# Performance work log

Measured on AMD Instinct MI355X. Metric: run time of the kernel, lower is better.

The kernel has to match this reference:

```python
import jax, jax.numpy as jnp
import numpy as np

B, S, D, H = 2, 2048, 1024, 16
DK = D // H


def setup_inputs() -> dict:
    key = jax.random.key(0)
    ks = jax.random.split(key, 11)
    scale = 1.0 / np.sqrt(D)
    inp = {
        "query": jax.random.normal(ks[0], (B, S, D), dtype=jnp.float32),
        "key": jax.random.normal(ks[1], (B, S, D), dtype=jnp.float32),
        "value": jax.random.normal(ks[2], (B, S, D), dtype=jnp.float32),
        "Wq": jax.random.normal(ks[3], (D, D), dtype=jnp.float32) * scale,
        "bq": jnp.zeros((D,), dtype=jnp.float32),
        "Wk": jax.random.normal(ks[4], (D, D), dtype=jnp.float32) * scale,
        "bk": jnp.zeros((D,), dtype=jnp.float32),
        "Wv": jax.random.normal(ks[5], (D, D), dtype=jnp.float32) * scale,
        "bv": jnp.zeros((D,), dtype=jnp.float32),
        "Wo": jax.random.normal(ks[6], (D, D), dtype=jnp.float32) * scale,
        "bo": jnp.zeros((D,), dtype=jnp.float32),
    }
    return inp


def _split_heads(x):
    # [B,S,D] -> [B,H,S,DK]
    b, s, _ = x.shape
    return x.reshape(b, s, H, DK).transpose(0, 2, 1, 3)


def reference(query, key, value, Wq, bq, Wk, bk, Wv, bv, Wo, bo):
    q = _split_heads(query @ Wq.T + bq)
    k = _split_heads(key @ Wk.T + bk)
    v = _split_heads(value @ Wv.T + bv)
    # scaled dot-product attention: [B,H,S,S]
    scores = jnp.einsum("bhqd,bhkd->bhqk", q, k) / np.sqrt(DK).astype(np.float32)
    attn = jax.nn.softmax(scores, axis=-1)  # stable max-subtract softmax, same math
    ctx = jnp.einsum("bhqk,bhkd->bhqd", attn, v)  # [B,H,S,DK]
    ctx = ctx.transpose(0, 2, 1, 3).reshape(query.shape[0], -1, H * DK)
    return ctx @ Wo.T + bo
```

## Files before the change

kernel.cpp:

```cpp
#include <hip/hip_runtime.h>
#include <math.h>

constexpr int NB = 2;
constexpr int NS = 2048;
constexpr int ND = 1024;
constexpr int NH = 16;
constexpr int NDK = 64;

typedef __attribute__((ext_vector_type(8))) short short8;
typedef __attribute__((ext_vector_type(4))) float floatx4;

__device__ inline unsigned short f2bf(float x) {
    unsigned u = __builtin_bit_cast(unsigned, x);
    u += 0x7fffu + ((u >> 16) & 1u);
    return (unsigned short)(u >> 16);
}

#define GLOAD_LDS16(g, l) __builtin_amdgcn_global_load_lds( \
    (const __attribute__((address_space(1))) void*)(g),     \
    (__attribute__((address_space(3))) void*)(l), 16, 0, 0)

#define QSCALE 0.18033688f

__global__ __launch_bounds__(256) void cvt3(
    const float* __restrict__ s0, const float* __restrict__ s1,
    const float* __restrict__ s2,
    unsigned short* __restrict__ d0, unsigned short* __restrict__ d1,
    unsigned short* __restrict__ d2)
{
    const float* s = (blockIdx.y == 0) ? s0 : (blockIdx.y == 1) ? s1 : s2;
    unsigned short* d = (blockIdx.y == 0) ? d0 : (blockIdx.y == 1) ? d1 : d2;
    int i = (blockIdx.x * 256 + threadIdx.x) * 8;
    float4 a = *(const float4*)(s + i);
    float4 b = *(const float4*)(s + i + 4);
    unsigned short t[8] = {f2bf(a.x), f2bf(a.y), f2bf(a.z), f2bf(a.w),
                           f2bf(b.x), f2bf(b.y), f2bf(b.z), f2bf(b.w)};
    *(uint4*)(d + i) = *(uint4*)t;
}

__global__ __launch_bounds__(256) void cvt4(
    const float* __restrict__ s0, const float* __restrict__ s1,
    const float* __restrict__ s2, const float* __restrict__ s3,
    unsigned short* __restrict__ d0, unsigned short* __restrict__ d1,
    unsigned short* __restrict__ d2, unsigned short* __restrict__ d3)
{
    const float* s = (blockIdx.y == 0) ? s0 : (blockIdx.y == 1) ? s1
                   : (blockIdx.y == 2) ? s2 : s3;
    unsigned short* d = (blockIdx.y == 0) ? d0 : (blockIdx.y == 1) ? d1
                      : (blockIdx.y == 2) ? d2 : d3;
    int i = (blockIdx.x * 256 + threadIdx.x) * 8;
    float4 a = *(const float4*)(s + i);
    float4 b = *(const float4*)(s + i + 4);
    unsigned short t[8] = {f2bf(a.x), f2bf(a.y), f2bf(a.z), f2bf(a.w),
                           f2bf(b.x), f2bf(b.y), f2bf(b.z), f2bf(b.w)};
    *(uint4*)(d + i) = *(uint4*)t;
}

#define BM 64
#define BN 128
#define BK 64

__global__ __launch_bounds__(256) void gemm_qkv(
    const unsigned short* __restrict__ Xq, const unsigned short* __restrict__ Xk,
    const unsigned short* __restrict__ Xv,
    const unsigned short* __restrict__ Wq, const unsigned short* __restrict__ Wk,
    const unsigned short* __restrict__ Wv,
    const float* __restrict__ bq, const float* __restrict__ bk,
    const float* __restrict__ bv,
    unsigned short* __restrict__ Cq, unsigned short* __restrict__ Ck,
    unsigned short* __restrict__ Cv)
{
    __shared__ unsigned short As[BM * BK];
    __shared__ unsigned short Bs[BN * BK];
    const int tid = threadIdx.x, w = tid >> 6, lane = tid & 63;
    const int lo = lane & 15, quad = lane >> 4;
    const int bid = blockIdx.x;
    const int seg = bid >> 9;
    const int wi  = bid & 511;
    const int K = ND;

    int bm, bn;
    const unsigned short *A, *Bw;
    const float* bias;
    if (seg == 2) { bn = wi & 31; bm = wi >> 5; A = Wv; Bw = Xv; bias = bv; }
    else if (seg == 1) { bn = wi & 7; bm = wi >> 3; A = Xk; Bw = Wk; bias = bk; }
    else { bn = wi & 7; bm = wi >> 3; A = Xq; Bw = Wq; bias = bq; }

    const int wm = (w >> 1) * 32, wn = (w & 1) * 64;

    const int ar0 = tid >> 3,            ag0 = (tid & 7) ^ (ar0 & 7);
    const int ar1 = (tid + 256) >> 3,    ag1 = (tid & 7) ^ (ar1 & 7);
    const unsigned short* Ag0 = A + (size_t)(bm * BM + ar0) * K + ag0 * 8;
    const unsigned short* Ag1 = A + (size_t)(bm * BM + ar1) * K + ag1 * 8;
    unsigned short* AsD0 = As + tid * 8;
    unsigned short* AsD1 = As + (tid + 256) * 8;

    const unsigned short* Bg[4];
    unsigned short* BsD[4];
    #pragma unroll
    for (int p = 0; p < 4; ++p) {
        int c = tid + 256 * p, r = c >> 3, g = (c & 7) ^ (r & 7);
        Bg[p] = Bw + (size_t)(bn * BN + r) * K + g * 8;
        BsD[p] = Bs + c * 8;
    }

    floatx4 acc[2][4];
    #pragma unroll
    for (int i = 0; i < 2; ++i)
        #pragma unroll
        for (int j = 0; j < 4; ++j) acc[i][j] = (floatx4){0.f, 0.f, 0.f, 0.f};

    for (int k0 = 0; k0 < K; k0 += BK) {
        GLOAD_LDS16(Ag0 + k0, AsD0);
        GLOAD_LDS16(Ag1 + k0, AsD1);
        #pragma unroll
        for (int p = 0; p < 4; ++p) GLOAD_LDS16(Bg[p] + k0, BsD[p]);
        __syncthreads();

        #pragma unroll
        for (int s = 0; s < 2; ++s) {
            const int pos = ((s * 4 + quad) ^ (lo & 7)) * 8;
            short8 af[2], bf[4];
            #pragma unroll
            for (int i = 0; i < 2; ++i)
                af[i] = *(const short8*)(As + (wm + i * 16 + lo) * BK + pos);
            #pragma unroll
            for (int j = 0; j < 4; ++j)
                bf[j] = *(const short8*)(Bs + (wn + j * 16 + lo) * BK + pos);
            #pragma unroll
            for (int i = 0; i < 2; ++i)
                #pragma unroll
                for (int j = 0; j < 4; ++j)
                    acc[i][j] = __builtin_amdgcn_mfma_f32_16x16x32_bf16(af[i], bf[j], acc[i][j], 0, 0, 0);
        }
        __syncthreads();
    }

    if (seg < 2) {
        unsigned short* C = seg ? Ck : Cq;
        const float scale = seg ? 1.f : QSCALE;
        #pragma unroll
        for (int j = 0; j < 4; ++j) {
            const int col = bn * BN + wn + j * 16 + lo;
            const float bb = bias[col];
            #pragma unroll
            for (int i = 0; i < 2; ++i)
                #pragma unroll
                for (int r = 0; r < 4; ++r) {
                    const int row = bm * BM + wm + i * 16 + quad * 4 + r;
                    C[(size_t)row * ND + col] = f2bf((acc[i][j][r] + bb) * scale);
                }
        }
    } else {
        #pragma unroll
        for (int i = 0; i < 2; ++i)
            #pragma unroll
            for (int r = 0; r < 4; ++r) {
                const int row = bm * BM + wm + i * 16 + quad * 4 + r;
                const float bb = bias[row];
                #pragma unroll
                for (int j = 0; j < 4; ++j) {
                    const int col = bn * BN + wn + j * 16 + lo;
                    const int b = col >> 11, s = col & (NS - 1);
                    Cv[(size_t)(b * ND + row) * NS + s] = f2bf(acc[i][j][r] + bb);
                }
            }
    }
}

__global__ __launch_bounds__(256) void gemm_o(
    const unsigned short* __restrict__ A, const unsigned short* __restrict__ Bw,
    const float* __restrict__ bias, float* __restrict__ Cout)
{
    __shared__ unsigned short As[BM * BK];
    __shared__ unsigned short Bs[BN * BK];
    const int tid = threadIdx.x, w = tid >> 6, lane = tid & 63;
    const int lo = lane & 15, quad = lane >> 4;
    const int bn = blockIdx.x, bm = blockIdx.y;
    const int K = ND;
    const int wm = (w >> 1) * 32, wn = (w & 1) * 64;

    const int ar0 = tid >> 3,            ag0 = (tid & 7) ^ (ar0 & 7);
    const int ar1 = (tid + 256) >> 3,    ag1 = (tid & 7) ^ (ar1 & 7);
    const unsigned short* Ag0 = A + (size_t)(bm * BM + ar0) * K + ag0 * 8;
    const unsigned short* Ag1 = A + (size_t)(bm * BM + ar1) * K + ag1 * 8;
    unsigned short* AsD0 = As + tid * 8;
    unsigned short* AsD1 = As + (tid + 256) * 8;

    const unsigned short* Bg[4];
    unsigned short* BsD[4];
    #pragma unroll
    for (int p = 0; p < 4; ++p) {
        int c = tid + 256 * p, r = c >> 3, g = (c & 7) ^ (r & 7);
        Bg[p] = Bw + (size_t)(bn * BN + r) * K + g * 8;
        BsD[p] = Bs + c * 8;
    }

    floatx4 acc[2][4];
    #pragma unroll
    for (int i = 0; i < 2; ++i)
        #pragma unroll
        for (int j = 0; j < 4; ++j) acc[i][j] = (floatx4){0.f, 0.f, 0.f, 0.f};

    for (int k0 = 0; k0 < K; k0 += BK) {
        GLOAD_LDS16(Ag0 + k0, AsD0);
        GLOAD_LDS16(Ag1 + k0, AsD1);
        #pragma unroll
        for (int p = 0; p < 4; ++p) GLOAD_LDS16(Bg[p] + k0, BsD[p]);
        __syncthreads();

        #pragma unroll
        for (int s = 0; s < 2; ++s) {
            const int pos = ((s * 4 + quad) ^ (lo & 7)) * 8;
            short8 af[2], bf[4];
            #pragma unroll
            for (int i = 0; i < 2; ++i)
                af[i] = *(const short8*)(As + (wm + i * 16 + lo) * BK + pos);
            #pragma unroll
            for (int j = 0; j < 4; ++j)
                bf[j] = *(const short8*)(Bs + (wn + j * 16 + lo) * BK + pos);
            #pragma unroll
            for (int i = 0; i < 2; ++i)
                #pragma unroll
                for (int j = 0; j < 4; ++j)
                    acc[i][j] = __builtin_amdgcn_mfma_f32_16x16x32_bf16(af[i], bf[j], acc[i][j], 0, 0, 0);
        }
        __syncthreads();
    }

    #pragma unroll
    for (int j = 0; j < 4; ++j) {
        const int col = bn * BN + wn + j * 16 + lo;
        const float bb = bias[col];
        #pragma unroll
        for (int i = 0; i < 2; ++i)
            #pragma unroll
            for (int r = 0; r < 4; ++r) {
                const int row = bm * BM + wm + i * 16 + quad * 4 + r;
                Cout[(size_t)row * ND + col] = acc[i][j][r] + bb;
            }
    }
}

constexpr int PRS = 72;

__global__ __launch_bounds__(256, 4) void attn_mfma(
    const unsigned short* __restrict__ qb,
    const unsigned short* __restrict__ kb,
    const unsigned short* __restrict__ vt,
    float* __restrict__ cacc,
    float* __restrict__ lbuf)
{
    __shared__ unsigned short Ks[64 * 64];
    __shared__ unsigned short Vs[64 * 64];
    __shared__ unsigned short Pt[4][32 * PRS];

    const int tid = threadIdx.x, w = tid >> 6, lane = tid & 63;
    const int lo = lane & 15, quad = lane >> 4;
    const int qgrp = blockIdx.x;
    const int ksp  = blockIdx.y;
    const int bh   = blockIdx.z;
    const int b = bh >> 4, h = bh & 15;
    const int q0 = qgrp * 128 + w * 32;

    short8 qf[2][2];
    #pragma unroll
    for (int qt = 0; qt < 2; ++qt) {
        const unsigned short* qrow =
            qb + (size_t)(b * NS + q0 + qt * 16 + lo) * ND + h * NDK + quad * 8;
        qf[qt][0] = *(const short8*)(qrow);
        qf[qt][1] = *(const short8*)(qrow + 32);
    }

    const int c0 = tid, c1 = tid + 256;
    const int r0 = c0 >> 3, g0 = (c0 & 7) ^ (r0 & 7);
    const int r1 = c1 >> 3, g1 = (c1 & 7) ^ (r1 & 7);
    const unsigned short* Ksrc0 = kb + (size_t)(b * NS + r0) * ND + h * NDK + g0 * 8;
    const unsigned short* Ksrc1 = kb + (size_t)(b * NS + r1) * ND + h * NDK + g1 * 8;
    const unsigned short* Vsrc0 = vt + (size_t)(bh * NDK + r0) * NS + g0 * 8;
    const unsigned short* Vsrc1 = vt + (size_t)(bh * NDK + r1) * NS + g1 * 8;
    unsigned short* Kd0 = Ks + c0 * 8;
    unsigned short* Kd1 = Ks + c1 * 8;
    unsigned short* Vd0 = Vs + c0 * 8;
    unsigned short* Vd1 = Vs + c1 * 8;

    floatx4 acc[2][4], lacc[2];
    #pragma unroll
    for (int qt = 0; qt < 2; ++qt) {
        lacc[qt] = (floatx4){0.f, 0.f, 0.f, 0.f};
        #pragma unroll
        for (int cb = 0; cb < 4; ++cb) acc[qt][cb] = (floatx4){0.f, 0.f, 0.f, 0.f};
    }

    const short8 ones = {0x3F80, 0x3F80, 0x3F80, 0x3F80,
                         0x3F80, 0x3F80, 0x3F80, 0x3F80};
    unsigned short* pw = &Pt[w][0];
    const int pos0 = (quad ^ (lo & 7)) * 8;
    const int pos1 = ((4 + quad) ^ (lo & 7)) * 8;

    for (int key0 = ksp * 1024; key0 < ksp * 1024 + 1024; key0 += 64) {
        GLOAD_LDS16(Ksrc0 + (size_t)key0 * ND, Kd0);
        GLOAD_LDS16(Ksrc1 + (size_t)key0 * ND, Kd1);
        GLOAD_LDS16(Vsrc0 + key0, Vd0);
        GLOAD_LDS16(Vsrc1 + key0, Vd1);
        __syncthreads();

        floatx4 s[2][4];
        #pragma unroll
        for (int t = 0; t < 4; ++t) {
            const int rw = (t * 16 + lo) * 64;
            const short8 kf0 = *(const short8*)(Ks + rw + pos0);
            const short8 kf1 = *(const short8*)(Ks + rw + pos1);
            #pragma unroll
            for (int qt = 0; qt < 2; ++qt) {
                s[qt][t] = __builtin_amdgcn_mfma_f32_16x16x32_bf16(
                    kf0, qf[qt][0], (floatx4){0.f, 0.f, 0.f, 0.f}, 0, 0, 0);
                s[qt][t] = __builtin_amdgcn_mfma_f32_16x16x32_bf16(
                    kf1, qf[qt][1], s[qt][t], 0, 0, 0);
            }
        }

        #pragma unroll
        for (int qt = 0; qt < 2; ++qt)
            #pragma unroll
            for (int t = 0; t < 4; ++t) {
                unsigned u0 = __builtin_bit_cast(unsigned, __builtin_amdgcn_exp2f(s[qt][t][0]));
                unsigned u1 = __builtin_bit_cast(unsigned, __builtin_amdgcn_exp2f(s[qt][t][1]));
                unsigned u2 = __builtin_bit_cast(unsigned, __builtin_amdgcn_exp2f(s[qt][t][2]));
                unsigned u3 = __builtin_bit_cast(unsigned, __builtin_amdgcn_exp2f(s[qt][t][3]));
                uint2 pk = {(u0 >> 16) | (u1 & 0xFFFF0000u),
                            (u2 >> 16) | (u3 & 0xFFFF0000u)};
                *(uint2*)(pw + (qt * 16 + lo) * PRS + t * 16 + quad * 4) = pk;
            }

        short8 pf[2][2];
        #pragma unroll
        for (int qt = 0; qt < 2; ++qt) {
            pf[qt][0] = *(const short8*)(pw + (qt * 16 + lo) * PRS + quad * 8);
            pf[qt][1] = *(const short8*)(pw + (qt * 16 + lo) * PRS + 32 + quad * 8);
            lacc[qt] = __builtin_amdgcn_mfma_f32_16x16x32_bf16(pf[qt][0], ones, lacc[qt], 0, 0, 0);
            lacc[qt] = __builtin_amdgcn_mfma_f32_16x16x32_bf16(pf[qt][1], ones, lacc[qt], 0, 0, 0);
        }

        #pragma unroll
        for (int cb = 0; cb < 4; ++cb) {
            const int rw = (cb * 16 + lo) * 64;
            const short8 vf0 = *(const short8*)(Vs + rw + pos0);
            const short8 vf1 = *(const short8*)(Vs + rw + pos1);
            #pragma unroll
            for (int qt = 0; qt < 2; ++qt) {
                acc[qt][cb] = __builtin_amdgcn_mfma_f32_16x16x32_bf16(pf[qt][0], vf0, acc[qt][cb], 0, 0, 0);
                acc[qt][cb] = __builtin_amdgcn_mfma_f32_16x16x32_bf16(pf[qt][1], vf1, acc[qt][cb], 0, 0, 0);
            }
        }
        __syncthreads();
    }

    #pragma unroll
    for (int qt = 0; qt < 2; ++qt) {
        #pragma unroll
        for (int cb = 0; cb < 4; ++cb)
            #pragma unroll
            for (int r = 0; r < 4; ++r) {
                size_t off = (size_t)(b * NS + q0 + qt * 16 + quad * 4 + r) * ND
                           + h * NDK + cb * 16 + lo;
                atomicAdd(&cacc[off], acc[qt][cb][r]);
            }
        if (lo == 0)
            #pragma unroll
            for (int r = 0; r < 4; ++r)
                atomicAdd(&lbuf[(size_t)bh * NS + q0 + qt * 16 + quad * 4 + r],
                          lacc[qt][r]);
    }
}

__global__ __launch_bounds__(256) void divide_ctx(
    const float* __restrict__ cacc, const float* __restrict__ lbuf,
    unsigned short* __restrict__ ctx)
{
    int idx = blockIdx.x * 256 + threadIdx.x;
    int base = idx * 8;
    int row = base >> 10;
    int col = base & 1023;
    int b = row >> 11, sq = row & 2047, h = col >> 6;
    float inv = 1.f / lbuf[(size_t)((b << 4) + h) * NS + sq];
    float4 a = *(const float4*)(cacc + base);
    float4 c = *(const float4*)(cacc + base + 4);
    unsigned short o[8] = {f2bf(a.x * inv), f2bf(a.y * inv), f2bf(a.z * inv), f2bf(a.w * inv),
                           f2bf(c.x * inv), f2bf(c.y * inv), f2bf(c.z * inv), f2bf(c.w * inv)};
    *(uint4*)(ctx + base) = *(uint4*)o;
}

extern "C" void kernel_launch(void* const* d_in, const int* in_sizes, int n_in,
                              void* d_out, int out_size, void* d_ws, size_t ws_size,
                              hipStream_t stream)
{
    const float* query = (const float*)d_in[0];
    const float* key   = (const float*)d_in[1];
    const float* value = (const float*)d_in[2];
    const float* Wq    = (const float*)d_in[3];
    const float* bq    = (const float*)d_in[4];
    const float* Wk    = (const float*)d_in[5];
    const float* bk    = (const float*)d_in[6];
    const float* Wv    = (const float*)d_in[7];
    const float* bv    = (const float*)d_in[8];
    const float* Wo    = (const float*)d_in[9];
    const float* bo    = (const float*)d_in[10];
    float* out = (float*)d_out;

    const size_t n  = (size_t)NB * NS * ND;
    const size_t nw = (size_t)ND * ND;

    unsigned short* X0   = (unsigned short*)d_ws;
    unsigned short* X1   = X0 + n;
    unsigned short* X2   = X1 + n;
    unsigned short* W0   = X2 + n;
    unsigned short* W1   = W0 + nw;
    unsigned short* W2   = W1 + nw;
    unsigned short* W3   = W2 + nw;
    unsigned short* qbuf = W3 + nw;
    unsigned short* kbuf = qbuf + n;
    unsigned short* vtb  = kbuf + n;
    float* lbuf = (float*)(vtb + n);
    float* cacc = (float*)X1;
    unsigned short* ctxb = qbuf;

    const int M = NB * NS;

    cvt3<<<dim3((int)(n  / 2048), 3), 256, 0, stream>>>(query, key, value, X0, X1, X2);
    cvt4<<<dim3((int)(nw / 2048), 4), 256, 0, stream>>>(Wq, Wk, Wv, Wo, W0, W1, W2, W3);

    gemm_qkv<<<1536, 256, 0, stream>>>(X0, X1, X2, W0, W1, W2,
                                       bq, bk, bv, qbuf, kbuf, vtb);

    hipMemsetAsync(cacc, 0, n * sizeof(float), stream);
    hipMemsetAsync(lbuf, 0, (size_t)NB * NH * NS * sizeof(float), stream);

    attn_mfma<<<dim3(NS / 128, 2, NB * NH), 256, 0, stream>>>(qbuf, kbuf, vtb, cacc, lbuf);

    divide_ctx<<<(int)(n / 8 / 256), 256, 0, stream>>>(cacc, lbuf, ctxb);

    gemm_o<<<dim3(ND / BN, M / BM), 256, 0, stream>>>(ctxb, W3, bo, out);
}
```

Baseline: 248.7 us.

## Merge conversion kernels, enlarge QKV GEMM tiles, replace attention atomics with split buffers

The two fp32-to-bf16 conversion launches are merged into one 7-way launch, with early exit for the smaller weight matrices. The QKV projection GEMM moves from 64x128x64 to 128x128x32 tiles so each block reuses more data, halving the block count. The attention kernel no longer atomically accumulates its two key-split partial results. Each split writes to its own context and row-sum buffers, which removes the two memsets and the atomics. The divide kernel sums the two partials, at the cost of an extra full-size fp32 buffer and more memory traffic in the divide step.

```diff
diff --git a/kernel.cpp b/kernel.cpp
--- a/kernel.cpp
+++ b/kernel.cpp
@@ -22,43 +22,30 @@
 
 #define QSCALE 0.18033688f
 
-__global__ __launch_bounds__(256) void cvt3(
+__global__ __launch_bounds__(256) void cvt_all(
     const float* __restrict__ s0, const float* __restrict__ s1,
-    const float* __restrict__ s2,
+    const float* __restrict__ s2, const float* __restrict__ s3,
+    const float* __restrict__ s4, const float* __restrict__ s5,
+    const float* __restrict__ s6,
     unsigned short* __restrict__ d0, unsigned short* __restrict__ d1,
-    unsigned short* __restrict__ d2)
-{
-    const float* s = (blockIdx.y == 0) ? s0 : (blockIdx.y == 1) ? s1 : s2;
-    unsigned short* d = (blockIdx.y == 0) ? d0 : (blockIdx.y == 1) ? d1 : d2;
+    unsigned short* __restrict__ d2, unsigned short* __restrict__ d3,
+    unsigned short* __restrict__ d4, unsigned short* __restrict__ d5,
+    unsigned short* __restrict__ d6)
+{
+    const int y = blockIdx.y;
+    const float* srcs[7] = {s0, s1, s2, s3, s4, s5, s6};
+    unsigned short* dsts[7] = {d0, d1, d2, d3, d4, d5, d6};
+    const int nel = (y < 3) ? NB * NS * ND : ND * ND;
     int i = (blockIdx.x * 256 + threadIdx.x) * 8;
+    if (i >= nel) return;
+    const float* s = srcs[y];
+    unsigned short* d = dsts[y];
     float4 a = *(const float4*)(s + i);
     float4 b = *(const float4*)(s + i + 4);
     unsigned short t[8] = {f2bf(a.x), f2bf(a.y), f2bf(a.z), f2bf(a.w),
                            f2bf(b.x), f2bf(b.y), f2bf(b.z), f2bf(b.w)};
     *(uint4*)(d + i) = *(uint4*)t;
 }
-
-__global__ __launch_bounds__(256) void cvt4(
-    const float* __restrict__ s0, const float* __restrict__ s1,
-    const float* __restrict__ s2, const float* __restrict__ s3,
-    unsigned short* __restrict__ d0, unsigned short* __restrict__ d1,
-    unsigned short* __restrict__ d2, unsigned short* __restrict__ d3)
-{
-    const float* s = (blockIdx.y == 0) ? s0 : (blockIdx.y == 1) ? s1
-                   : (blockIdx.y == 2) ? s2 : s3;
-    unsigned short* d = (blockIdx.y == 0) ? d0 : (blockIdx.y == 1) ? d1
-                      : (blockIdx.y == 2) ? d2 : d3;
-    int i = (blockIdx.x * 256 + threadIdx.x) * 8;
-    float4 a = *(const float4*)(s + i);
-    float4 b = *(const float4*)(s + i + 4);
-    unsigned short t[8] = {f2bf(a.x), f2bf(a.y), f2bf(a.z), f2bf(a.w),
-                           f2bf(b.x), f2bf(b.y), f2bf(b.z), f2bf(b.w)};
-    *(uint4*)(d + i) = *(uint4*)t;
-}
-
-#define BM 64
-#define BN 128
-#define BK 64
 
 __global__ __launch_bounds__(256) void gemm_qkv(
     const unsigned short* __restrict__ Xq, const unsigned short* __restrict__ Xk,
@@ -70,28 +57,114 @@
     unsigned short* __restrict__ Cq, unsigned short* __restrict__ Ck,
     unsigned short* __restrict__ Cv)
 {
-    __shared__ unsigned short As[BM * BK];
-    __shared__ unsigned short Bs[BN * BK];
+    __shared__ unsigned short As[128 * 32];
+    __shared__ unsigned short Bs[128 * 32];
     const int tid = threadIdx.x, w = tid >> 6, lane = tid & 63;
     const int lo = lane & 15, quad = lane >> 4;
     const int bid = blockIdx.x;
-    const int seg = bid >> 9;
-    const int wi  = bid & 511;
+    const int seg = bid >> 8;
+    const int wi  = bid & 255;
     const int K = ND;
 
     int bm, bn;
     const unsigned short *A, *Bw;
     const float* bias;
-    if (seg == 2) { bn = wi & 31; bm = wi >> 5; A = Wv; Bw = Xv; bias = bv; }
-    else if (seg == 1) { bn = wi & 7; bm = wi >> 3; A = Xk; Bw = Wk; bias = bk; }
-    else { bn = wi & 7; bm = wi >> 3; A = Xq; Bw = Wq; bias = bq; }
-
+    if (seg == 2)      { bn = wi & 31; bm = wi >> 5; A = Wv; Bw = Xv; bias = bv; }
+    else if (seg == 1) { bn = wi & 7;  bm = wi >> 3; A = Xk; Bw = Wk; bias = bk; }
+    else               { bn = wi & 7;  bm = wi >> 3; A = Xq; Bw = Wq; bias = bq; }
+
+    const int wm = (w >> 1) * 64, wn = (w & 1) * 64;
+
+    const int srow = tid >> 2;
+    const int sch = (tid & 3) ^ (srow & 3);
+    const unsigned short* Ag0 = A + (size_t)(bm * 128 + srow) * K + sch * 8;
+    const unsigned short* Ag1 = Ag0 + (size_t)64 * K;
+    const unsigned short* Bg0 = Bw + (size_t)(bn * 128 + srow) * K + sch * 8;
+    const unsigned short* Bg1 = Bg0 + (size_t)64 * K;
+    unsigned short* AsD0 = As + tid * 8;
+    unsigned short* AsD1 = As + (tid + 256) * 8;
+    unsigned short* BsD0 = Bs + tid * 8;
+    unsigned short* BsD1 = Bs + (tid + 256) * 8;
+
+    floatx4 acc[4][4];
+    #pragma unroll
+    for (int i = 0; i < 4; ++i)
+        #pragma unroll
+        for (int j = 0; j < 4; ++j) acc[i][j] = (floatx4){0.f, 0.f, 0.f, 0.f};
+
+    const int rpos = (quad ^ (lo & 3)) * 8;
+
+    for (int k0 = 0; k0 < K; k0 += 32) {
+        GLOAD_LDS16(Ag0 + k0, AsD0);
+        GLOAD_LDS16(Ag1 + k0, AsD1);
+        GLOAD_LDS16(Bg0 + k0, BsD0);
+        GLOAD_LDS16(Bg1 + k0, BsD1);
+        __syncthreads();
+
+        short8 af[4], bf[4];
+        #pragma unroll
+        for (int i = 0; i < 4; ++i)
+            af[i] = *(const short8*)(As + (wm + i * 16 + lo) * 32 + rpos);
+        #pragma unroll
+        for (int j = 0; j < 4; ++j)
+            bf[j] = *(const short8*)(Bs + (wn + j * 16 + lo) * 32 + rpos);
+
+        #pragma unroll
+        for (int i = 0; i < 4; ++i)
+            #pragma unroll
+            for (int j = 0; j < 4; ++j)
+                acc[i][j] = __builtin_amdgcn_mfma_f32_16x16x32_bf16(af[i], bf[j], acc[i][j], 0, 0, 0);
+        __syncthreads();
+    }
+
+    if (seg < 2) {
+        unsigned short* C = seg ? Ck : Cq;
+        const float scale = seg ? 1.f : QSCALE;
+        #pragma unroll
+        for (int j = 0; j < 4; ++j) {
+            const int col = bn * 128 + wn + j * 16 + lo;
+            const float bb = bias[col];
+            #pragma unroll
+            for (int i = 0; i < 4; ++i)
+                #pragma unroll
+                for (int r = 0; r < 4; ++r) {
+                    const int row = bm * 128 + wm + i * 16 + quad * 4 + r;
+                    C[(size_t)row * ND + col] = f2bf((acc[i][j][r] + bb) * scale);
+                }
+        }
+    } else {
+        #pragma unroll
+        for (int i = 0; i < 4; ++i)
+            #pragma unroll
+            for (int r = 0; r < 4; ++r) {
+                const int row = bm * 128 + wm + i * 16 + quad * 4 + r;
+                const float bb = bias[row];
+                #pragma unroll
+                for (int j = 0; j < 4; ++j) {
+                    const int col = bn * 128 + wn + j * 16 + lo;
+                    const int b = col >> 11, s = col & (NS - 1);
+                    Cv[(size_t)(b * ND + row) * NS + s] = f2bf(acc[i][j][r] + bb);
+                }
+            }
+    }
+}
+
+__global__ __launch_bounds__(256) void gemm_o(
+    const unsigned short* __restrict__ A, const unsigned short* __restrict__ Bw,
+    const float* __restrict__ bias, float* __restrict__ Cout)
+{
+    __shared__ unsigned short As[64 * 64];
+    __shared__ unsigned short Bs[128 * 64];
+    const int tid = threadIdx.x, w = tid >> 6, lane = tid & 63;
+    const int lo = lane & 15, quad = lane >> 4;
+    const int bn = blockIdx.x, bm = blockIdx.y;
+    const int K = ND;
     const int wm = (w >> 1) * 32, wn = (w & 1) * 64;
 
     const int ar0 = tid >> 3,            ag0 = (tid & 7) ^ (ar0 & 7);
     const int ar1 = (tid + 256) >> 3,    ag1 = (tid & 7) ^ (ar1 & 7);
-    const unsigned short* Ag0 = A + (size_t)(bm * BM + ar0) * K + ag0 * 8;
-    const unsigned short* Ag1 = A + (size_t)(bm * BM + ar1) * K + ag1 * 8;
+    const unsigned short* Ag0 = A + (size_t)(bm * 64 + ar0) * K + ag0 * 8;
+    const unsigned short* Ag1 = A + (size_t)(bm * 64 + ar1) * K + ag1 * 8;
     unsigned short* AsD0 = As + tid * 8;
     unsigned short* AsD1 = As + (tid + 256) * 8;
 
@@ -100,7 +173,7 @@
     #pragma unroll
     for (int p = 0; p < 4; ++p) {
         int c = tid + 256 * p, r = c >> 3, g = (c & 7) ^ (r & 7);
-        Bg[p] = Bw + (size_t)(bn * BN + r) * K + g * 8;
+        Bg[p] = Bw + (size_t)(bn * 128 + r) * K + g * 8;
         BsD[p] = Bs + c * 8;
     }
 
@@ -110,7 +183,7 @@
         #pragma unroll
         for (int j = 0; j < 4; ++j) acc[i][j] = (floatx4){0.f, 0.f, 0.f, 0.f};
 
-    for (int k0 = 0; k0 < K; k0 += BK) {
+    for (int k0 = 0; k0 < K; k0 += 64) {
         GLOAD_LDS16(Ag0 + k0, AsD0);
         GLOAD_LDS16(Ag1 + k0, AsD1);
         #pragma unroll
@@ -123,10 +196,10 @@
             short8 af[2], bf[4];
             #pragma unroll
             for (int i = 0; i < 2; ++i)
-                af[i] = *(const short8*)(As + (wm + i * 16 + lo) * BK + pos);
+                af[i] = *(const short8*)(As + (wm + i * 16 + lo) * 64 + pos);
             #pragma unroll
             for (int j = 0; j < 4; ++j)
-                bf[j] = *(const short8*)(Bs + (wn + j * 16 + lo) * BK + pos);
+                bf[j] = *(const short8*)(Bs + (wn + j * 16 + lo) * 64 + pos);
             #pragma unroll
             for (int i = 0; i < 2; ++i)
                 #pragma unroll
@@ -136,107 +209,15 @@
         __syncthreads();
     }
 
-    if (seg < 2) {
-        unsigned short* C = seg ? Ck : Cq;
-        const float scale = seg ? 1.f : QSCALE;
-        #pragma unroll
-        for (int j = 0; j < 4; ++j) {
-            const int col = bn * BN + wn + j * 16 + lo;
-            const float bb = bias[col];
-            #pragma unroll
-            for (int i = 0; i < 2; ++i)
-                #pragma unroll
-                for (int r = 0; r < 4; ++r) {
-                    const int row = bm * BM + wm + i * 16 + quad * 4 + r;
-                    C[(size_t)row * ND + col] = f2bf((acc[i][j][r] + bb) * scale);
-                }
-        }
-    } else {
+    #pragma unroll
+    for (int j = 0; j < 4; ++j) {
+        const int col = bn * 128 + wn + j * 16 + lo;
+        const float bb = bias[col];
         #pragma unroll
         for (int i = 0; i < 2; ++i)
             #pragma unroll
             for (int r = 0; r < 4; ++r) {
-                const int row = bm * BM + wm + i * 16 + quad * 4 + r;
-                const float bb = bias[row];
-                #pragma unroll
-                for (int j = 0; j < 4; ++j) {
-                    const int col = bn * BN + wn + j * 16 + lo;
-                    const int b = col >> 11, s = col & (NS - 1);
-                    Cv[(size_t)(b * ND + row) * NS + s] = f2bf(acc[i][j][r] + bb);
-                }
-            }
-    }
-}
-
-__global__ __launch_bounds__(256) void gemm_o(
-    const unsigned short* __restrict__ A, const unsigned short* __restrict__ Bw,
-    const float* __restrict__ bias, float* __restrict__ Cout)
-{
-    __shared__ unsigned short As[BM * BK];
-    __shared__ unsigned short Bs[BN * BK];
-    const int tid = threadIdx.x, w = tid >> 6, lane = tid & 63;
-    const int lo = lane & 15, quad = lane >> 4;
-    const int bn = blockIdx.x, bm = blockIdx.y;
-    const int K = ND;
-    const int wm = (w >> 1) * 32, wn = (w & 1) * 64;
-
-    const int ar0 = tid >> 3,            ag0 = (tid & 7) ^ (ar0 & 7);
-    const int ar1 = (tid + 256) >> 3,    ag1 = (tid & 7) ^ (ar1 & 7);
-    const unsigned short* Ag0 = A + (size_t)(bm * BM + ar0) * K + ag0 * 8;
-    const unsigned short* Ag1 = A + (size_t)(bm * BM + ar1) * K + ag1 * 8;
-    unsigned short* AsD0 = As + tid * 8;
-    unsigned short* AsD1 = As + (tid + 256) * 8;
-
-    const unsigned short* Bg[4];
-    unsigned short* BsD[4];
-    #pragma unroll
-    for (int p = 0; p < 4; ++p) {
-        int c = tid + 256 * p, r = c >> 3, g = (c & 7) ^ (r & 7);
-        Bg[p] = Bw + (size_t)(bn * BN + r) * K + g * 8;
-        BsD[p] = Bs + c * 8;
-    }
-
-    floatx4 acc[2][4];
-    #pragma unroll
-    for (int i = 0; i < 2; ++i)
-        #pragma unroll
-        for (int j = 0; j < 4; ++j) acc[i][j] = (floatx4){0.f, 0.f, 0.f, 0.f};
-
-    for (int k0 = 0; k0 < K; k0 += BK) {
-        GLOAD_LDS16(Ag0 + k0, AsD0);
-        GLOAD_LDS16(Ag1 + k0, AsD1);
-        #pragma unroll
-        for (int p = 0; p < 4; ++p) GLOAD_LDS16(Bg[p] + k0, BsD[p]);
-        __syncthreads();
-
-        #pragma unroll
-        for (int s = 0; s < 2; ++s) {
-            const int pos = ((s * 4 + quad) ^ (lo & 7)) * 8;
-            short8 af[2], bf[4];
-            #pragma unroll
-            for (int i = 0; i < 2; ++i)
-                af[i] = *(const short8*)(As + (wm + i * 16 + lo) * BK + pos);
-            #pragma unroll
-            for (int j = 0; j < 4; ++j)
-                bf[j] = *(const short8*)(Bs + (wn + j * 16 + lo) * BK + pos);
-            #pragma unroll
-            for (int i = 0; i < 2; ++i)
-                #pragma unroll
-                for (int j = 0; j < 4; ++j)
-                    acc[i][j] = __builtin_amdgcn_mfma_f32_16x16x32_bf16(af[i], bf[j], acc[i][j], 0, 0, 0);
-        }
-        __syncthreads();
-    }
-
-    #pragma unroll
-    for (int j = 0; j < 4; ++j) {
-        const int col = bn * BN + wn + j * 16 + lo;
-        const float bb = bias[col];
-        #pragma unroll
-        for (int i = 0; i < 2; ++i)
-            #pragma unroll
-            for (int r = 0; r < 4; ++r) {
-                const int row = bm * BM + wm + i * 16 + quad * 4 + r;
+                const int row = bm * 64 + wm + i * 16 + quad * 4 + r;
                 Cout[(size_t)row * ND + col] = acc[i][j][r] + bb;
             }
     }
@@ -248,7 +229,7 @@
     const unsigned short* __restrict__ qb,
     const unsigned short* __restrict__ kb,
     const unsigned short* __restrict__ vt,
-    float* __restrict__ cacc,
+    float* __restrict__ cacc0, float* __restrict__ cacc1,
     float* __restrict__ lbuf)
 {
     __shared__ unsigned short Ks[64 * 64];
@@ -356,6 +337,8 @@
         __syncthreads();
     }
 
+    float* ca = ksp ? cacc1 : cacc0;
+    float* lb = lbuf + (size_t)ksp * (NB * NH * NS);
     #pragma unroll
     for (int qt = 0; qt < 2; ++qt) {
         #pragma unroll
@@ -364,30 +347,35 @@
             for (int r = 0; r < 4; ++r) {
                 size_t off = (size_t)(b * NS + q0 + qt * 16 + quad * 4 + r) * ND
                            + h * NDK + cb * 16 + lo;
-                atomicAdd(&cacc[off], acc[qt][cb][r]);
+                ca[off] = acc[qt][cb][r];
             }
         if (lo == 0)
             #pragma unroll
             for (int r = 0; r < 4; ++r)
-                atomicAdd(&lbuf[(size_t)bh * NS + q0 + qt * 16 + quad * 4 + r],
-                          lacc[qt][r]);
+                lb[(size_t)bh * NS + q0 + qt * 16 + quad * 4 + r] = lacc[qt][r];
     }
 }
 
 __global__ __launch_bounds__(256) void divide_ctx(
-    const float* __restrict__ cacc, const float* __restrict__ lbuf,
-    unsigned short* __restrict__ ctx)
+    const float* __restrict__ cacc0, const float* __restrict__ cacc1,
+    const float* __restrict__ lbuf, unsigned short* __restrict__ ctx)
 {
     int idx = blockIdx.x * 256 + threadIdx.x;
     int base = idx * 8;
     int row = base >> 10;
     int col = base & 1023;
     int b = row >> 11, sq = row & 2047, h = col >> 6;
-    float inv = 1.f / lbuf[(size_t)((b << 4) + h) * NS + sq];
-    float4 a = *(const float4*)(cacc + base);
-    float4 c = *(const float4*)(cacc + base + 4);
-    unsigned short o[8] = {f2bf(a.x * inv), f2bf(a.y * inv), f2bf(a.z * inv), f2bf(a.w * inv),
-                           f2bf(c.x * inv), f2bf(c.y * inv), f2bf(c.z * inv), f2bf(c.w * inv)};
+    size_t li = (size_t)((b << 4) + h) * NS + sq;
+    float inv = 1.f / (lbuf[li] + lbuf[li + (size_t)NB * NH * NS]);
+    float4 a0 = *(const float4*)(cacc0 + base);
+    float4 a1 = *(const float4*)(cacc0 + base + 4);
+    float4 c0 = *(const float4*)(cacc1 + base);
+    float4 c1 = *(const float4*)(cacc1 + base + 4);
+    unsigned short o[8] = {
+        f2bf((a0.x + c0.x) * inv), f2bf((a0.y + c0.y) * inv),
+        f2bf((a0.z + c0.z) * inv), f2bf((a0.w + c0.w) * inv),
+        f2bf((a1.x + c1.x) * inv), f2bf((a1.y + c1.y) * inv),
+        f2bf((a1.z + c1.z) * inv), f2bf((a1.w + c1.w) * inv)};
     *(uint4*)(ctx + base) = *(uint4*)o;
 }
 
@@ -421,24 +409,23 @@
     unsigned short* qbuf = W3 + nw;
     unsigned short* kbuf = qbuf + n;
     unsigned short* vtb  = kbuf + n;
-    float* lbuf = (float*)(vtb + n);
-    float* cacc = (float*)X1;
+    float* cacc1 = (float*)(vtb + n);
+    float* lbuf  = cacc1 + n;
+    float* cacc0 = (float*)X1;
     unsigned short* ctxb = qbuf;
 
     const int M = NB * NS;
 
-    cvt3<<<dim3((int)(n  / 2048), 3), 256, 0, stream>>>(query, key, value, X0, X1, X2);
-    cvt4<<<dim3((int)(nw / 2048), 4), 256, 0, stream>>>(Wq, Wk, Wv, Wo, W0, W1, W2, W3);
-
-    gemm_qkv<<<1536, 256, 0, stream>>>(X0, X1, X2, W0, W1, W2,
-                                       bq, bk, bv, qbuf, kbuf, vtb);
-
-    hipMemsetAsync(cacc, 0, n * sizeof(float), stream);
-    hipMemsetAsync(lbuf, 0, (size_t)NB * NH * NS * sizeof(float), stream);
-
-    attn_mfma<<<dim3(NS / 128, 2, NB * NH), 256, 0, stream>>>(qbuf, kbuf, vtb, cacc, lbuf);
-
-    divide_ctx<<<(int)(n / 8 / 256), 256, 0, stream>>>(cacc, lbuf, ctxb);
-
-    gemm_o<<<dim3(ND / BN, M / BM), 256, 0, stream>>>(ctxb, W3, bo, out);
-}
+    cvt_all<<<dim3((int)(n / 2048), 7), 256, 0, stream>>>(
+        query, key, value, Wq, Wk, Wv, Wo, X0, X1, X2, W0, W1, W2, W3);
+
+    gemm_qkv<<<768, 256, 0, stream>>>(X0, X1, X2, W0, W1, W2,
+                                      bq, bk, bv, qbuf, kbuf, vtb);
+
+    attn_mfma<<<dim3(NS / 128, 2, NB * NH), 256, 0, stream>>>(
+        qbuf, kbuf, vtb, cacc0, cacc1, lbuf);
+
+    divide_ctx<<<(int)(n / 8 / 256), 256, 0, stream>>>(cacc0, cacc1, lbuf, ctxb);
+
+    gemm_o<<<dim3(ND / 128, M / 64), 256, 0, stream>>>(ctxb, W3, bo, out);
+}
```

Result: faster. 234.4 us (-5.7%).
